# Performance work log

Hardware: AMD Instinct MI355X
Metric: run time of the kernel (lower is better)

The kernel has to match this reference:

```python
import jax, jax.numpy as jnp
import numpy as np

NH = 8  # n_heads

def ln(x, g, b, eps=1e-5):
    m = x.mean(-1, keepdims=True)
    v = ((x - m) ** 2).mean(-1, keepdims=True)
    return (x - m) / jnp.sqrt(v + eps) * g + b

def setup_inputs() -> dict:
    key0 = jax.random.key(0)
    ks = jax.random.split(key0, 16)
    B, C, F, H = 4, 8, 2048, 512
    Hf = 2 * H
    s = 0.02
    return {
        'query': jax.random.normal(ks[0], (B, F, H), jnp.float32),
        'key': jax.random.normal(ks[1], (B, C, F, H), jnp.float32),
        'value': jax.random.normal(ks[2], (B, C, F, H), jnp.float32),
        'Wq': jax.random.normal(ks[3], (H, H), jnp.float32) * s,
        'bq': jnp.zeros((H,), jnp.float32),
        'Wk': jax.random.normal(ks[4], (H, H), jnp.float32) * s,
        'bk': jnp.zeros((H,), jnp.float32),
        'Wv': jax.random.normal(ks[5], (H, H), jnp.float32) * s,
        'bv': jnp.zeros((H,), jnp.float32),
        'Wo': jax.random.normal(ks[6], (H, H), jnp.float32) * s,
        'bo': jnp.zeros((H,), jnp.float32),
        'ln1_g': jnp.ones((H,), jnp.float32),
        'ln1_b': jnp.zeros((H,), jnp.float32),
        'W1': jax.random.normal(ks[7], (Hf, H), jnp.float32) * s,
        'b1': jnp.zeros((Hf,), jnp.float32),
        'W2': jax.random.normal(ks[8], (H, Hf), jnp.float32) * s,
        'b2': jnp.zeros((H,), jnp.float32),
        'ln2_g': jnp.ones((H,), jnp.float32),
        'ln2_b': jnp.zeros((H,), jnp.float32),
    }

def reference(query, key, value, Wq, bq, Wk, bk, Wv, bv, Wo, bo,
              ln1_g, ln1_b, W1, b1, W2, b2, ln2_g, ln2_b):
    B0, F0, H = query.shape
    # faithful to the original torch reshapes (pure reinterpretation, not permute)
    q = query.reshape(F0, B0, 1, H)                                   # [F,B,1,H]
    k = key.reshape(key.shape[2], key.shape[0], key.shape[1], key.shape[3])    # [F,B,C,H]
    v = value.reshape(value.shape[2], value.shape[0], value.shape[1], value.shape[3])
    dh = H // NH
    def heads(x):
        f, b, s, _ = x.shape
        return x.reshape(f, b, s, NH, dh).transpose(0, 1, 3, 2, 4)    # [F,B,nh,S,dh]
    Q = heads(q @ Wq.T + bq)
    K = heads(k @ Wk.T + bk)
    V = heads(v @ Wv.T + bv)
    scale = jnp.sqrt(jnp.float32(dh))
    att = jax.nn.softmax(jnp.einsum('fbhqd,fbhkd->fbhqk', Q, K) / scale, axis=-1)
    x = jnp.einsum('fbhqk,fbhkd->fbhqd', att, V)                      # [F,B,nh,1,dh]
    x = x.transpose(0, 1, 3, 2, 4).reshape(F0, B0, -1, H)
    x = x @ Wo.T + bo
    h1 = ln(q + x, ln1_g, ln1_b)                                      # residual + LN
    ff = jax.nn.relu(h1 @ W1.T + b1) @ W2.T + b2                      # FFN (dropout=eval identity)
    out = ln(h1 + ff, ln2_g, ln2_b)                                   # [F,B,1,H]
    return out.reshape(B0, F0, H)
```

## Files before the change

### kernel.cpp

```cpp
#include <hip/hip_runtime.h>
#include <cstdint>
#include <cstddef>

#define DEVFN static __device__ __forceinline__

typedef __attribute__((ext_vector_type(4))) float f32x4;
typedef __attribute__((ext_vector_type(8))) __bf16 bf16x8;

typedef __attribute__((address_space(1))) void gvoid;
typedef __attribute__((address_space(3))) void svoid;

DEVFN unsigned short f32_to_bf16_bits(float f) {
  uint32_t u = __builtin_bit_cast(uint32_t, f);
  return (unsigned short)((u + 0x7fffu + ((u >> 16) & 1u)) >> 16);
}
DEVFN float bf16_lo(uint32_t d) {
  return __builtin_bit_cast(float, d << 16);
}
DEVFN float bf16_hi(uint32_t d) {
  return __builtin_bit_cast(float, d & 0xffff0000u);
}
DEVFN uint32_t pack_bf16x2(float lo, float hi) {
  return (uint32_t)f32_to_bf16_bits(lo) | ((uint32_t)f32_to_bf16_bits(hi) << 16);
}

DEVFN void load_lds16(const void* g, void* l) {
  __builtin_amdgcn_global_load_lds((const gvoid*)g, (svoid*)l, 16, 0, 0);
}

__global__ __launch_bounds__(256) void cvt_all(
    const float* __restrict__ q, const float* __restrict__ Wq,
    const float* __restrict__ Wv, const float* __restrict__ Wo,
    const float* __restrict__ W1, const float* __restrict__ W2,
    unsigned short* __restrict__ qb, unsigned short* __restrict__ Wqb,
    unsigned short* __restrict__ Wvb, unsigned short* __restrict__ Wob,
    unsigned short* __restrict__ W1b, unsigned short* __restrict__ W2b) {
  int i = (int)(blockIdx.x * 256 + threadIdx.x);
  const float* src;
  unsigned short* dst;
  int off;
  if (i < 524288)      { src = q;  dst = qb;  off = i; }
  else if (i < 557056) { src = Wq; dst = Wqb; off = i - 524288; }
  else if (i < 589824) { src = Wv; dst = Wvb; off = i - 557056; }
  else if (i < 622592) { src = Wo; dst = Wob; off = i - 589824; }
  else if (i < 688128) { src = W1; dst = W1b; off = i - 622592; }
  else                 { src = W2; dst = W2b; off = i - 688128; }
  const float4* p = (const float4*)src;
  float4 a = p[2 * off], b = p[2 * off + 1];
  union { unsigned short s[8]; uint4 v; } o;
  o.s[0] = f32_to_bf16_bits(a.x); o.s[1] = f32_to_bf16_bits(a.y);
  o.s[2] = f32_to_bf16_bits(a.z); o.s[3] = f32_to_bf16_bits(a.w);
  o.s[4] = f32_to_bf16_bits(b.x); o.s[5] = f32_to_bf16_bits(b.y);
  o.s[6] = f32_to_bf16_bits(b.z); o.s[7] = f32_to_bf16_bits(b.w);
  ((uint4*)dst)[off] = o.v;
}

__global__ __launch_bounds__(256) void wkt_kernel(const float* __restrict__ Wk,
                                                  unsigned short* __restrict__ WkT) {
  int idx = (int)(blockIdx.x * 256 + threadIdx.x);
  int d = idx & 63;
  int j = (idx >> 6) & 511;
  int h = idx >> 15;
  WkT[idx] = f32_to_bf16_bits(Wk[((h << 6) + d) * 512 + j]);
}

template<int BN, bool OUT_BF16, bool RELU, bool ADD_RES>
__global__ __launch_bounds__(256)
void gemm_bt(const unsigned short* __restrict__ A, int lda, long long zA,
             const unsigned short* __restrict__ Bt, int ldb, long long zB,
             void* __restrict__ Cv, int ldc, long long zC,
             const float* __restrict__ bias, int zBias,
             const float* __restrict__ res, int ldres,
             int K) {
  constexpr int BM = 128;
  constexpr int WN = BN / 2;
  constexpr int NT = WN / 16;
  __shared__ __align__(16) unsigned short As[BM * 32];
  __shared__ __align__(16) unsigned short Bs[BN * 32];

  const int tid = (int)threadIdx.x;
  const int lane = tid & 63;
  const int w = tid >> 6;
  const int wm = w >> 1;
  const int wn = w & 1;
  const int m0 = (int)blockIdx.y * BM;
  const int n0 = (int)blockIdx.x * BN;
  const long long z = (long long)blockIdx.z;

  A += z * zA;
  Bt += z * zB;
  const float* biasz = bias ? (bias + z * zBias) : nullptr;

  f32x4 acc[4][NT];
#pragma unroll
  for (int i = 0; i < 4; ++i)
#pragma unroll
    for (int j = 0; j < NT; ++j) acc[i][j] = f32x4{0.f, 0.f, 0.f, 0.f};

  const int o0 = w * 1024 + lane * 16;
  const int r0 = o0 >> 6, c0 = (o0 & 63) >> 1;
  const int o1 = o0 + 4096;
  const int r1 = o1 >> 6, c1 = (o1 & 63) >> 1;

  const int kIters = K / 32;
  for (int kt = 0; kt < kIters; ++kt) {
    const int k0 = kt * 32;
    __syncthreads();
    load_lds16(A + (size_t)(m0 + r0) * lda + (k0 + c0), As + w * 512);
    load_lds16(A + (size_t)(m0 + r1) * lda + (k0 + c1), As + 2048 + w * 512);
    if (BN == 128) {
      load_lds16(Bt + (size_t)(n0 + r0) * ldb + (k0 + c0), Bs + w * 512);
      load_lds16(Bt + (size_t)(n0 + r1) * ldb + (k0 + c1), Bs + 2048 + w * 512);
    } else {
      load_lds16(Bt + (size_t)(n0 + r0) * ldb + (k0 + c0), Bs + w * 512);
    }
    asm volatile("s_waitcnt vmcnt(0)" ::: "memory");
    __syncthreads();

    const int fr = lane & 15;
    const int kq = lane >> 4;
    bf16x8 af[4], bf[NT];
#pragma unroll
    for (int i = 0; i < 4; ++i) {
      const int m = wm * 64 + i * 16 + fr;
      af[i] = __builtin_bit_cast(bf16x8, *(const uint4*)(As + m * 32 + kq * 8));
    }
#pragma unroll
    for (int j = 0; j < NT; ++j) {
      const int n = wn * WN + j * 16 + fr;
      bf[j] = __builtin_bit_cast(bf16x8, *(const uint4*)(Bs + n * 32 + kq * 8));
    }
#pragma unroll
    for (int i = 0; i < 4; ++i)
#pragma unroll
      for (int j = 0; j < NT; ++j)
        acc[i][j] = __builtin_amdgcn_mfma_f32_16x16x32_bf16(af[i], bf[j], acc[i][j], 0, 0, 0);
  }

  const int fr = lane & 15;
  const int rq = lane >> 4;
  unsigned short* Cb = (unsigned short*)Cv + z * zC;
  float* Cf = (float*)Cv + z * zC;
#pragma unroll
  for (int i = 0; i < 4; ++i) {
    const int rbase = m0 + wm * 64 + i * 16 + rq * 4;
#pragma unroll
    for (int j = 0; j < NT; ++j) {
      const int col = n0 + wn * WN + j * 16 + fr;
      const float bvv = biasz ? biasz[col] : 0.f;
#pragma unroll
      for (int r = 0; r < 4; ++r) {
        float v = acc[i][j][r] + bvv;
        if (ADD_RES) v += res[(size_t)(rbase + r) * ldres + col];
        if (RELU) v = fmaxf(v, 0.f);
        if (OUT_BF16) Cb[(size_t)(rbase + r) * ldc + col] = f32_to_bf16_bits(v);
        else Cf[(size_t)(rbase + r) * ldc + col] = v;
      }
    }
  }
}

__global__ __launch_bounds__(256) void attn_kernel(const float* __restrict__ key,
                                                   const float* __restrict__ value,
                                                   unsigned short* __restrict__ U) {
  extern __shared__ float smem[];
  const int tid = (int)threadIdx.x;
  const int lane = tid & 63;
  const int w = tid >> 6;
  const int n0 = (int)blockIdx.x * 8;

  auto issue = [&](int n, int buf) {
    const float* kg = key + (size_t)n * 4096;
    const float* vg = value + (size_t)n * 4096;
    float* kl = smem + buf * 8192;
    float* vl = kl + 4096;
#pragma unroll
    for (int j = 0; j < 4; ++j) {
      const int o = w * 1024 + j * 256;
      load_lds16(kg + o + lane * 4, kl + o);
      load_lds16(vg + o + lane * 4, vl + o);
    }
  };

  issue(n0, 0);

  for (int i = 0; i < 8; ++i) {
    asm volatile("s_waitcnt vmcnt(0)" ::: "memory");
    __syncthreads();
    if (i < 7) issue(n0 + i + 1, (i + 1) & 1);

    const float* kf = smem + (i & 1) * 8192;
    const float* vf = kf + 4096;
    uint32_t* Un32 = (uint32_t*)(U + (size_t)(n0 + i) * 4096);

#pragma unroll
    for (int hh = 0; hh < 2; ++hh) {
      const int h = w * 2 + hh;
      uint2 ud0 = *(const uint2*)(Un32 + h * 256 + lane * 2);
      uint2 ud1 = *(const uint2*)(Un32 + h * 256 + 128 + lane * 2);
      float u[8] = {bf16_lo(ud0.x), bf16_hi(ud0.x), bf16_lo(ud0.y), bf16_hi(ud0.y),
                    bf16_lo(ud1.x), bf16_hi(ud1.x), bf16_lo(ud1.y), bf16_hi(ud1.y)};

      float zc[8];
      float zmax = -1e30f;
#pragma unroll
      for (int c = 0; c < 8; ++c) {
        float4 k0 = *(const float4*)(kf + c * 512 + lane * 4);
        float4 k1 = *(const float4*)(kf + c * 512 + 256 + lane * 4);
        float p = u[0] * k0.x + u[1] * k0.y + u[2] * k0.z + u[3] * k0.w +
                  u[4] * k1.x + u[5] * k1.y + u[6] * k1.z + u[7] * k1.w;
#pragma unroll
        for (int off = 32; off > 0; off >>= 1) p += __shfl_xor(p, off, 64);
        zc[c] = p * 0.125f;
        zmax = fmaxf(zmax, zc[c]);
      }
      float se = 0.f;
#pragma unroll
      for (int c = 0; c < 8; ++c) { zc[c] = __expf(zc[c] - zmax); se += zc[c]; }
      const float inv = 1.f / se;
#pragma unroll
      for (int c = 0; c < 8; ++c) zc[c] *= inv;

      float a[8] = {0.f, 0.f, 0.f, 0.f, 0.f, 0.f, 0.f, 0.f};
#pragma unroll
      for (int c = 0; c < 8; ++c) {
        float4 v0 = *(const float4*)(vf + c * 512 + lane * 4);
        float4 v1 = *(const float4*)(vf + c * 512 + 256 + lane * 4);
        a[0] += zc[c] * v0.x; a[1] += zc[c] * v0.y;
        a[2] += zc[c] * v0.z; a[3] += zc[c] * v0.w;
        a[4] += zc[c] * v1.x; a[5] += zc[c] * v1.y;
        a[6] += zc[c] * v1.z; a[7] += zc[c] * v1.w;
      }
      uint2 s0, s1;
      s0.x = pack_bf16x2(a[0], a[1]); s0.y = pack_bf16x2(a[2], a[3]);
      s1.x = pack_bf16x2(a[4], a[5]); s1.y = pack_bf16x2(a[6], a[7]);
      *(uint2*)(Un32 + h * 256 + lane * 2) = s0;
      *(uint2*)(Un32 + h * 256 + 128 + lane * 2) = s1;
    }
  }
}

__global__ __launch_bounds__(256) void ln_kernel(const float* __restrict__ in,
                                                 const float* __restrict__ g,
                                                 const float* __restrict__ b,
                                                 float* __restrict__ outf,
                                                 unsigned short* __restrict__ outb) {
  const int lane = (int)threadIdx.x & 63;
  const size_t row = (size_t)blockIdx.x * 4 + (threadIdx.x >> 6);
  const int col = lane * 8;
  const float* x = in + row * 512;
  float4 a0 = *(const float4*)(x + col);
  float4 a1 = *(const float4*)(x + col + 4);
  float v[8] = {a0.x, a0.y, a0.z, a0.w, a1.x, a1.y, a1.z, a1.w};
  float s = 0.f, sq = 0.f;
#pragma unroll
  for (int t = 0; t < 8; ++t) { s += v[t]; sq += v[t] * v[t]; }
#pragma unroll
  for (int off = 32; off > 0; off >>= 1) {
    s += __shfl_xor(s, off, 64);
    sq += __shfl_xor(sq, off, 64);
  }
  const float mean = s * (1.f / 512.f);
  const float var = sq * (1.f / 512.f) - mean * mean;
  const float rstd = rsqrtf(var + 1e-5f);
  float o[8];
#pragma unroll
  for (int t = 0; t < 8; ++t) o[t] = (v[t] - mean) * rstd * g[col + t] + b[col + t];
  if (outf) {
    *(float4*)(outf + row * 512 + col) = make_float4(o[0], o[1], o[2], o[3]);
    *(float4*)(outf + row * 512 + col + 4) = make_float4(o[4], o[5], o[6], o[7]);
  }
  if (outb) {
    union { unsigned short s_[8]; uint4 v_; } u;
#pragma unroll
    for (int t = 0; t < 8; ++t) u.s_[t] = f32_to_bf16_bits(o[t]);
    *(uint4*)(outb + row * 512 + col) = u.v_;
  }
}

extern "C" void kernel_launch(void* const* d_in, const int* in_sizes, int n_in,
                              void* d_out, int out_size, void* d_ws, size_t ws_size,
                              hipStream_t stream) {
  const float* query = (const float*)d_in[0];
  const float* key   = (const float*)d_in[1];
  const float* value = (const float*)d_in[2];
  const float* Wq = (const float*)d_in[3];
  const float* bq = (const float*)d_in[4];
  const float* Wk = (const float*)d_in[5];
  const float* Wv = (const float*)d_in[7];
  const float* bv = (const float*)d_in[8];
  const float* Wo = (const float*)d_in[9];
  const float* bo = (const float*)d_in[10];
  const float* ln1g = (const float*)d_in[11];
  const float* ln1b = (const float*)d_in[12];
  const float* W1 = (const float*)d_in[13];
  const float* b1 = (const float*)d_in[14];
  const float* W2 = (const float*)d_in[15];
  const float* b2 = (const float*)d_in[16];
  const float* ln2g = (const float*)d_in[17];
  const float* ln2b = (const float*)d_in[18];
  float* out = (float*)d_out;

  char* ws = (char*)d_ws;
  size_t off = 0;
  auto alloc = [&](size_t bytes) -> void* {
    off = (off + 255) & ~(size_t)255;
    void* p = ws + off;
    off += bytes;
    return p;
  };

  const int N = 8192;
  unsigned short* qb   = (unsigned short*)alloc((size_t)N * 512 * 2);
  unsigned short* Wqb  = (unsigned short*)alloc(512 * 512 * 2);
  unsigned short* Wvb  = (unsigned short*)alloc(512 * 512 * 2);
  unsigned short* Wob  = (unsigned short*)alloc(512 * 512 * 2);
  unsigned short* W1b  = (unsigned short*)alloc(1024 * 512 * 2);
  unsigned short* W2b  = (unsigned short*)alloc(512 * 1024 * 2);
  unsigned short* WkT  = (unsigned short*)alloc(8 * 512 * 64 * 2);
  unsigned short* Qp   = (unsigned short*)alloc((size_t)N * 512 * 2);
  unsigned short* U    = (unsigned short*)alloc((size_t)N * 4096 * 2);
  float*          h1pre= (float*)alloc((size_t)N * 512 * 4);
  unsigned short* h1b  = (unsigned short*)alloc((size_t)N * 512 * 2);
  float*          h1f  = (float*)alloc((size_t)N * 512 * 4);
  unsigned short* mid  = (unsigned short*)alloc((size_t)N * 1024 * 2);
  unsigned short* x    = Qp;
  float*          o2pre= h1pre;
  (void)ws_size; (void)in_sizes; (void)n_in; (void)out_size;

  dim3 blk(256);
  cvt_all<<<2944, blk, 0, stream>>>(query, Wq, Wv, Wo, W1, W2,
                                    qb, Wqb, Wvb, Wob, W1b, W2b);
  wkt_kernel<<<1024, blk, 0, stream>>>(Wk, WkT);

  gemm_bt<128, true, false, false><<<dim3(4, 64, 1), blk, 0, stream>>>(
      qb, 512, 0, Wqb, 512, 0, Qp, 512, 0, bq, 0, nullptr, 0, 512);
  gemm_bt<128, true, false, false><<<dim3(4, 64, 8), blk, 0, stream>>>(
      Qp, 512, 64, WkT, 64, 32768, U, 4096, 512, nullptr, 0, nullptr, 0, 64);
  attn_kernel<<<1024, blk, 65536, stream>>>(key, value, U);
  gemm_bt<64, true, false, false><<<dim3(1, 64, 8), blk, 0, stream>>>(
      U, 4096, 512, Wvb, 512, 32768, x, 512, 64, bv, 64, nullptr, 0, 512);
  gemm_bt<128, false, false, true><<<dim3(4, 64, 1), blk, 0, stream>>>(
      x, 512, 0, Wob, 512, 0, h1pre, 512, 0, bo, 0, query, 512, 512);
  ln_kernel<<<2048, blk, 0, stream>>>(h1pre, ln1g, ln1b, h1f, h1b);
  gemm_bt<128, true, true, false><<<dim3(8, 64, 1), blk, 0, stream>>>(
      h1b, 512, 0, W1b, 512, 0, mid, 1024, 0, b1, 0, nullptr, 0, 512);
  gemm_bt<128, false, false, true><<<dim3(4, 64, 1), blk, 0, stream>>>(
      mid, 1024, 0, W2b, 1024, 0, o2pre, 512, 0, b2, 0, h1f, 512, 1024);
  ln_kernel<<<2048, blk, 0, stream>>>(o2pre, ln2g, ln2b, out, nullptr);
}
```

Baseline: 560.2 us.

## Fuse Wk transpose into convert, shrink GEMM tiles, rewrite attention per-wave

The separate Wk transpose kernel is merged into the conversion kernel, removing one launch. The GEMMs gain a BM template parameter and most launches switch to 64x64 tiles, giving more blocks for the small M=8192 problems. The attention kernel is rewritten so each wave handles one position across all 8 heads, reading key/value directly from global memory instead of staging them through double-buffered LDS. The aim is better occupancy and fewer shuffle rounds per head, at the cost of more registers per thread and less reuse per GEMM tile.

```diff
diff --git a/kernel.cpp b/kernel.cpp
--- a/kernel.cpp
+++ b/kernel.cpp
@@ -14,12 +14,8 @@
   uint32_t u = __builtin_bit_cast(uint32_t, f);
   return (unsigned short)((u + 0x7fffu + ((u >> 16) & 1u)) >> 16);
 }
-DEVFN float bf16_lo(uint32_t d) {
-  return __builtin_bit_cast(float, d << 16);
-}
-DEVFN float bf16_hi(uint32_t d) {
-  return __builtin_bit_cast(float, d & 0xffff0000u);
-}
+DEVFN float bf16_lo(uint32_t d) { return __builtin_bit_cast(float, d << 16); }
+DEVFN float bf16_hi(uint32_t d) { return __builtin_bit_cast(float, d & 0xffff0000u); }
 DEVFN uint32_t pack_bf16x2(float lo, float hi) {
   return (uint32_t)f32_to_bf16_bits(lo) | ((uint32_t)f32_to_bf16_bits(hi) << 16);
 }
@@ -32,10 +28,25 @@
     const float* __restrict__ q, const float* __restrict__ Wq,
     const float* __restrict__ Wv, const float* __restrict__ Wo,
     const float* __restrict__ W1, const float* __restrict__ W2,
+    const float* __restrict__ Wk,
     unsigned short* __restrict__ qb, unsigned short* __restrict__ Wqb,
     unsigned short* __restrict__ Wvb, unsigned short* __restrict__ Wob,
-    unsigned short* __restrict__ W1b, unsigned short* __restrict__ W2b) {
+    unsigned short* __restrict__ W1b, unsigned short* __restrict__ W2b,
+    unsigned short* __restrict__ WkT) {
   int i = (int)(blockIdx.x * 256 + threadIdx.x);
+  if (i >= 753664) {
+    int off = i - 753664;
+    int oidx = off * 8;
+    int d0 = oidx & 63;
+    int j = (oidx >> 6) & 511;
+    int h = oidx >> 15;
+    union { unsigned short s[8]; uint4 v; } o;
+#pragma unroll
+    for (int t = 0; t < 8; ++t)
+      o.s[t] = f32_to_bf16_bits(Wk[(size_t)((h << 6) + d0 + t) * 512 + j]);
+    ((uint4*)WkT)[off] = o.v;
+    return;
+  }
   const float* src;
   unsigned short* dst;
   int off;
@@ -55,16 +66,7 @@
   ((uint4*)dst)[off] = o.v;
 }
 
-__global__ __launch_bounds__(256) void wkt_kernel(const float* __restrict__ Wk,
-                                                  unsigned short* __restrict__ WkT) {
-  int idx = (int)(blockIdx.x * 256 + threadIdx.x);
-  int d = idx & 63;
-  int j = (idx >> 6) & 511;
-  int h = idx >> 15;
-  WkT[idx] = f32_to_bf16_bits(Wk[((h << 6) + d) * 512 + j]);
-}
-
-template<int BN, bool OUT_BF16, bool RELU, bool ADD_RES>
+template<int BM, int BN, bool OUT_BF16, bool RELU, bool ADD_RES>
 __global__ __launch_bounds__(256)
 void gemm_bt(const unsigned short* __restrict__ A, int lda, long long zA,
              const unsigned short* __restrict__ Bt, int ldb, long long zB,
@@ -72,9 +74,10 @@
              const float* __restrict__ bias, int zBias,
              const float* __restrict__ res, int ldres,
              int K) {
-  constexpr int BM = 128;
-  constexpr int WN = BN / 2;
-  constexpr int NT = WN / 16;
+  constexpr int MT = BM / 32;
+  constexpr int NT = BN / 32;
+  constexpr int AQ = BM / 64;
+  constexpr int BQ = BN / 64;
   __shared__ __align__(16) unsigned short As[BM * 32];
   __shared__ __align__(16) unsigned short Bs[BN * 32];
 
@@ -91,47 +94,52 @@
   Bt += z * zB;
   const float* biasz = bias ? (bias + z * zBias) : nullptr;
 
-  f32x4 acc[4][NT];
-#pragma unroll
-  for (int i = 0; i < 4; ++i)
+  f32x4 acc[MT][NT];
+#pragma unroll
+  for (int i = 0; i < MT; ++i)
 #pragma unroll
     for (int j = 0; j < NT; ++j) acc[i][j] = f32x4{0.f, 0.f, 0.f, 0.f};
 
-  const int o0 = w * 1024 + lane * 16;
-  const int r0 = o0 >> 6, c0 = (o0 & 63) >> 1;
-  const int o1 = o0 + 4096;
-  const int r1 = o1 >> 6, c1 = (o1 & 63) >> 1;
+  int rA[AQ], cA[AQ], rB[BQ], cB[BQ];
+#pragma unroll
+  for (int q = 0; q < AQ; ++q) {
+    const int o = q * 4096 + w * 1024 + lane * 16;
+    rA[q] = o >> 6; cA[q] = (o & 63) >> 1;
+  }
+#pragma unroll
+  for (int q = 0; q < BQ; ++q) {
+    const int o = q * 4096 + w * 1024 + lane * 16;
+    rB[q] = o >> 6; cB[q] = (o & 63) >> 1;
+  }
 
   const int kIters = K / 32;
   for (int kt = 0; kt < kIters; ++kt) {
     const int k0 = kt * 32;
     __syncthreads();
-    load_lds16(A + (size_t)(m0 + r0) * lda + (k0 + c0), As + w * 512);
-    load_lds16(A + (size_t)(m0 + r1) * lda + (k0 + c1), As + 2048 + w * 512);
-    if (BN == 128) {
-      load_lds16(Bt + (size_t)(n0 + r0) * ldb + (k0 + c0), Bs + w * 512);
-      load_lds16(Bt + (size_t)(n0 + r1) * ldb + (k0 + c1), Bs + 2048 + w * 512);
-    } else {
-      load_lds16(Bt + (size_t)(n0 + r0) * ldb + (k0 + c0), Bs + w * 512);
-    }
+#pragma unroll
+    for (int q = 0; q < AQ; ++q)
+      load_lds16(A + (size_t)(m0 + rA[q]) * lda + (k0 + cA[q]), As + q * 2048 + w * 512);
+#pragma unroll
+    for (int q = 0; q < BQ; ++q)
+      load_lds16(Bt + (size_t)(n0 + rB[q]) * ldb + (k0 + cB[q]), Bs + q * 2048 + w * 512);
     asm volatile("s_waitcnt vmcnt(0)" ::: "memory");
     __syncthreads();
 
     const int fr = lane & 15;
     const int kq = lane >> 4;
-    bf16x8 af[4], bf[NT];
-#pragma unroll
-    for (int i = 0; i < 4; ++i) {
-      const int m = wm * 64 + i * 16 + fr;
+    bf16x8 af[MT], bf[NT];
+#pragma unroll
+    for (int i = 0; i < MT; ++i) {
+      const int m = wm * (BM / 2) + i * 16 + fr;
       af[i] = __builtin_bit_cast(bf16x8, *(const uint4*)(As + m * 32 + kq * 8));
     }
 #pragma unroll
     for (int j = 0; j < NT; ++j) {
-      const int n = wn * WN + j * 16 + fr;
+      const int n = wn * (BN / 2) + j * 16 + fr;
       bf[j] = __builtin_bit_cast(bf16x8, *(const uint4*)(Bs + n * 32 + kq * 8));
     }
 #pragma unroll
-    for (int i = 0; i < 4; ++i)
+    for (int i = 0; i < MT; ++i)
 #pragma unroll
       for (int j = 0; j < NT; ++j)
         acc[i][j] = __builtin_amdgcn_mfma_f32_16x16x32_bf16(af[i], bf[j], acc[i][j], 0, 0, 0);
@@ -142,11 +150,11 @@
   unsigned short* Cb = (unsigned short*)Cv + z * zC;
   float* Cf = (float*)Cv + z * zC;
 #pragma unroll
-  for (int i = 0; i < 4; ++i) {
-    const int rbase = m0 + wm * 64 + i * 16 + rq * 4;
+  for (int i = 0; i < MT; ++i) {
+    const int rbase = m0 + wm * (BM / 2) + i * 16 + rq * 4;
 #pragma unroll
     for (int j = 0; j < NT; ++j) {
-      const int col = n0 + wn * WN + j * 16 + fr;
+      const int col = n0 + wn * (BN / 2) + j * 16 + fr;
       const float bvv = biasz ? biasz[col] : 0.f;
 #pragma unroll
       for (int r = 0; r < 4; ++r) {
@@ -163,80 +171,83 @@
 __global__ __launch_bounds__(256) void attn_kernel(const float* __restrict__ key,
                                                    const float* __restrict__ value,
                                                    unsigned short* __restrict__ U) {
-  extern __shared__ float smem[];
-  const int tid = (int)threadIdx.x;
-  const int lane = tid & 63;
-  const int w = tid >> 6;
-  const int n0 = (int)blockIdx.x * 8;
-
-  auto issue = [&](int n, int buf) {
-    const float* kg = key + (size_t)n * 4096;
-    const float* vg = value + (size_t)n * 4096;
-    float* kl = smem + buf * 8192;
-    float* vl = kl + 4096;
-#pragma unroll
-    for (int j = 0; j < 4; ++j) {
-      const int o = w * 1024 + j * 256;
-      load_lds16(kg + o + lane * 4, kl + o);
-      load_lds16(vg + o + lane * 4, vl + o);
-    }
-  };
-
-  issue(n0, 0);
-
-  for (int i = 0; i < 8; ++i) {
-    asm volatile("s_waitcnt vmcnt(0)" ::: "memory");
-    __syncthreads();
-    if (i < 7) issue(n0 + i + 1, (i + 1) & 1);
-
-    const float* kf = smem + (i & 1) * 8192;
-    const float* vf = kf + 4096;
-    uint32_t* Un32 = (uint32_t*)(U + (size_t)(n0 + i) * 4096);
-
-#pragma unroll
-    for (int hh = 0; hh < 2; ++hh) {
-      const int h = w * 2 + hh;
-      uint2 ud0 = *(const uint2*)(Un32 + h * 256 + lane * 2);
-      uint2 ud1 = *(const uint2*)(Un32 + h * 256 + 128 + lane * 2);
-      float u[8] = {bf16_lo(ud0.x), bf16_hi(ud0.x), bf16_lo(ud0.y), bf16_hi(ud0.y),
-                    bf16_lo(ud1.x), bf16_hi(ud1.x), bf16_lo(ud1.y), bf16_hi(ud1.y)};
-
-      float zc[8];
-      float zmax = -1e30f;
-#pragma unroll
-      for (int c = 0; c < 8; ++c) {
-        float4 k0 = *(const float4*)(kf + c * 512 + lane * 4);
-        float4 k1 = *(const float4*)(kf + c * 512 + 256 + lane * 4);
-        float p = u[0] * k0.x + u[1] * k0.y + u[2] * k0.z + u[3] * k0.w +
-                  u[4] * k1.x + u[5] * k1.y + u[6] * k1.z + u[7] * k1.w;
-#pragma unroll
-        for (int off = 32; off > 0; off >>= 1) p += __shfl_xor(p, off, 64);
-        zc[c] = p * 0.125f;
-        zmax = fmaxf(zmax, zc[c]);
-      }
-      float se = 0.f;
-#pragma unroll
-      for (int c = 0; c < 8; ++c) { zc[c] = __expf(zc[c] - zmax); se += zc[c]; }
-      const float inv = 1.f / se;
-#pragma unroll
-      for (int c = 0; c < 8; ++c) zc[c] *= inv;
-
-      float a[8] = {0.f, 0.f, 0.f, 0.f, 0.f, 0.f, 0.f, 0.f};
-#pragma unroll
-      for (int c = 0; c < 8; ++c) {
-        float4 v0 = *(const float4*)(vf + c * 512 + lane * 4);
-        float4 v1 = *(const float4*)(vf + c * 512 + 256 + lane * 4);
-        a[0] += zc[c] * v0.x; a[1] += zc[c] * v0.y;
-        a[2] += zc[c] * v0.z; a[3] += zc[c] * v0.w;
-        a[4] += zc[c] * v1.x; a[5] += zc[c] * v1.y;
-        a[6] += zc[c] * v1.z; a[7] += zc[c] * v1.w;
-      }
-      uint2 s0, s1;
-      s0.x = pack_bf16x2(a[0], a[1]); s0.y = pack_bf16x2(a[2], a[3]);
-      s1.x = pack_bf16x2(a[4], a[5]); s1.y = pack_bf16x2(a[6], a[7]);
-      *(uint2*)(Un32 + h * 256 + lane * 2) = s0;
-      *(uint2*)(Un32 + h * 256 + 128 + lane * 2) = s1;
-    }
+  const int lane = (int)threadIdx.x & 63;
+  const int n = (int)blockIdx.x * 4 + ((int)threadIdx.x >> 6);
+
+  const uint4* Uq = (const uint4*)(U + (size_t)n * 4096);
+  float u[8][8];
+#pragma unroll
+  for (int h = 0; h < 8; ++h) {
+    uint4 d = Uq[h * 64 + lane];
+    u[h][0] = bf16_lo(d.x); u[h][1] = bf16_hi(d.x);
+    u[h][2] = bf16_lo(d.y); u[h][3] = bf16_hi(d.y);
+    u[h][4] = bf16_lo(d.z); u[h][5] = bf16_hi(d.z);
+    u[h][6] = bf16_lo(d.w); u[h][7] = bf16_hi(d.w);
+  }
+
+  float zc[8][8];
+#pragma unroll
+  for (int c = 0; c < 8; ++c) {
+    const float4* kp = (const float4*)(key + ((size_t)n * 8 + c) * 512);
+    float4 k0 = kp[lane * 2];
+    float4 k1 = kp[lane * 2 + 1];
+    float p[8];
+#pragma unroll
+    for (int h = 0; h < 8; ++h) {
+      p[h] = u[h][0] * k0.x + u[h][1] * k0.y + u[h][2] * k0.z + u[h][3] * k0.w +
+             u[h][4] * k1.x + u[h][5] * k1.y + u[h][6] * k1.z + u[h][7] * k1.w;
+    }
+#pragma unroll
+    for (int off = 1; off < 64; off <<= 1) {
+#pragma unroll
+      for (int h = 0; h < 8; ++h) p[h] += __shfl_xor(p[h], off, 64);
+    }
+#pragma unroll
+    for (int h = 0; h < 8; ++h) zc[h][c] = p[h] * 0.125f;
+  }
+
+#pragma unroll
+  for (int h = 0; h < 8; ++h) {
+    float m = zc[h][0];
+#pragma unroll
+    for (int c = 1; c < 8; ++c) m = fmaxf(m, zc[h][c]);
+    float se = 0.f;
+#pragma unroll
+    for (int c = 0; c < 8; ++c) { zc[h][c] = __expf(zc[h][c] - m); se += zc[h][c]; }
+    const float inv = 1.f / se;
+#pragma unroll
+    for (int c = 0; c < 8; ++c) zc[h][c] *= inv;
+  }
+
+  float acc[8][8];
+#pragma unroll
+  for (int h = 0; h < 8; ++h)
+#pragma unroll
+    for (int t = 0; t < 8; ++t) acc[h][t] = 0.f;
+#pragma unroll
+  for (int c = 0; c < 8; ++c) {
+    const float4* vp = (const float4*)(value + ((size_t)n * 8 + c) * 512);
+    float4 v0 = vp[lane * 2];
+    float4 v1 = vp[lane * 2 + 1];
+#pragma unroll
+    for (int h = 0; h < 8; ++h) {
+      const float a = zc[h][c];
+      acc[h][0] += a * v0.x; acc[h][1] += a * v0.y;
+      acc[h][2] += a * v0.z; acc[h][3] += a * v0.w;
+      acc[h][4] += a * v1.x; acc[h][5] += a * v1.y;
+      acc[h][6] += a * v1.z; acc[h][7] += a * v1.w;
+    }
+  }
+
+  uint4* Uw = (uint4*)(U + (size_t)n * 4096);
+#pragma unroll
+  for (int h = 0; h < 8; ++h) {
+    uint4 o;
+    o.x = pack_bf16x2(acc[h][0], acc[h][1]);
+    o.y = pack_bf16x2(acc[h][2], acc[h][3]);
+    o.z = pack_bf16x2(acc[h][4], acc[h][5]);
+    o.w = pack_bf16x2(acc[h][6], acc[h][7]);
+    Uw[h * 64 + lane] = o;
   }
 }
 
@@ -329,23 +340,22 @@
   (void)ws_size; (void)in_sizes; (void)n_in; (void)out_size;
 
   dim3 blk(256);
-  cvt_all<<<2944, blk, 0, stream>>>(query, Wq, Wv, Wo, W1, W2,
-                                    qb, Wqb, Wvb, Wob, W1b, W2b);
-  wkt_kernel<<<1024, blk, 0, stream>>>(Wk, WkT);
-
-  gemm_bt<128, true, false, false><<<dim3(4, 64, 1), blk, 0, stream>>>(
+  cvt_all<<<3072, blk, 0, stream>>>(query, Wq, Wv, Wo, W1, W2, Wk,
+                                    qb, Wqb, Wvb, Wob, W1b, W2b, WkT);
+
+  gemm_bt<64, 64, true, false, false><<<dim3(8, 128, 1), blk, 0, stream>>>(
       qb, 512, 0, Wqb, 512, 0, Qp, 512, 0, bq, 0, nullptr, 0, 512);
-  gemm_bt<128, true, false, false><<<dim3(4, 64, 8), blk, 0, stream>>>(
+  gemm_bt<128, 128, true, false, false><<<dim3(4, 64, 8), blk, 0, stream>>>(
       Qp, 512, 64, WkT, 64, 32768, U, 4096, 512, nullptr, 0, nullptr, 0, 64);
-  attn_kernel<<<1024, blk, 65536, stream>>>(key, value, U);
-  gemm_bt<64, true, false, false><<<dim3(1, 64, 8), blk, 0, stream>>>(
+  attn_kernel<<<2048, blk, 0, stream>>>(key, value, U);
+  gemm_bt<64, 64, true, false, false><<<dim3(1, 128, 8), blk, 0, stream>>>(
       U, 4096, 512, Wvb, 512, 32768, x, 512, 64, bv, 64, nullptr, 0, 512);
-  gemm_bt<128, false, false, true><<<dim3(4, 64, 1), blk, 0, stream>>>(
+  gemm_bt<64, 64, false, false, true><<<dim3(8, 128, 1), blk, 0, stream>>>(
       x, 512, 0, Wob, 512, 0, h1pre, 512, 0, bo, 0, query, 512, 512);
   ln_kernel<<<2048, blk, 0, stream>>>(h1pre, ln1g, ln1b, h1f, h1b);
-  gemm_bt<128, true, true, false><<<dim3(8, 64, 1), blk, 0, stream>>>(
+  gemm_bt<64, 64, true, true, false><<<dim3(16, 128, 1), blk, 0, stream>>>(
       h1b, 512, 0, W1b, 512, 0, mid, 1024, 0, b1, 0, nullptr, 0, 512);
-  gemm_bt<128, false, false, true><<<dim3(4, 64, 1), blk, 0, stream>>>(
+  gemm_bt<64, 64, false, false, true><<<dim3(8, 128, 1), blk, 0, stream>>>(
       mid, 1024, 0, W2b, 1024, 0, o2pre, 512, 0, b2, 0, h1f, 512, 1024);
   ln_kernel<<<2048, blk, 0, stream>>>(o2pre, ln2g, ln2b, out, nullptr);
 }
```

New measurement: 505.0 us. -9.8%, faster.
